# Optimization experiments

Hardware: AMD Instinct MI355X
Metric: run time of the kernel (lower is better)

## Reference

```python
import jax, jax.numpy as jnp
import numpy as np

# Channel layout assumed by the model's CH dict
CH_ELEV, CH_WS, CH_WD, CH_HUM, CH_NDVI, CH_FIRE = 0, 1, 2, 3, 4, 5
P_BURN, W_WIND, W_SLOPE = 0.58, 0.045, 0.078
OFFSETS = [(-1, 0), (-1, 1), (0, 1), (1, 1), (1, 0), (1, -1), (0, -1), (-1, -1)]
DIR_ANGLES = [90.0, 45.0, 0.0, 315.0, 270.0, 225.0, 180.0, 135.0]
SOBEL_X = np.array([[-1, 0, 1], [-2, 0, 2], [-1, 0, 1]], np.float32) / 8.0
SOBEL_Y = np.array([[-1, -2, -1], [0, 0, 0], [1, 2, 1]], np.float32) / 8.0


def setup_inputs() -> dict:
    key = jax.random.key(0)
    x = jax.random.uniform(key, (16, 6, 1024, 1024), dtype=jnp.float32)
    return {"x": x}


def _conv2d_same(img, k):
    # img: (B,1,H,W), k: (3,3)
    kern = jnp.asarray(k).reshape(1, 1, 3, 3)
    return jax.lax.conv_general_dilated(img, kern, (1, 1), ((1, 1), (1, 1)))


def _shift(mask, dr, dc):
    # mask: (B,H,W) float; zero-padded shift matching torch slicing
    B, H, W = mask.shape
    p = jnp.pad(mask, ((0, 0), (1, 1), (1, 1)))
    return p[:, 1 + dr:1 + dr + H, 1 + dc:1 + dc + W]


def reference(x):
    B, C, H, W = x.shape
    elev = x[:, CH_ELEV:CH_ELEV + 1]          # (B,1,H,W)
    ws = x[:, CH_WS]                           # (B,H,W)
    wd = x[:, CH_WD]
    hum = x[:, CH_HUM]
    ndvi = x[:, CH_NDVI]
    fs = x[:, CH_FIRE]

    dx = _conv2d_same(elev, SOBEL_X)
    dy = _conv2d_same(elev, SOBEL_Y)
    grad_mag = jnp.sqrt(dx * dx + dy * dy + 1e-8)
    slope = (jnp.arctan(grad_mag) * (180.0 / np.pi))[:, 0]  # (B,H,W) degrees

    burning = (fs > 0.5).astype(x.dtype)
    wind_math = jnp.mod(270.0 - wd, 360.0)
    slope_effect = 1.0 + W_SLOPE * jnp.tan(slope * (np.pi / 180.0))
    moisture_damp = jnp.clip(1.0 - 2.0 * hum * 200.0, 0.3, 1.0)
    veg_factor = 0.5 + 0.5 * jnp.clip(ndvi, 0.0, 1.0)
    base = P_BURN * slope_effect * moisture_damp * veg_factor  # wind-independent part

    prob = jnp.zeros((B, H, W), dtype=x.dtype)
    for (dr, dc), d_angle in zip(OFFSETS, DIR_ANGLES):
        shifted = _shift(burning, dr, dc)
        angle_diff = (d_angle - wind_math) * (np.pi / 180.0)
        wind_factor = 1.0 + W_WIND * jnp.cos(angle_diff) * ws
        p_spread = jnp.clip(base * wind_factor, 0.0, 1.0)
        prob = jnp.maximum(prob, shifted * p_spread)

    unburned = (fs < 0.5).astype(x.dtype)
    out = jnp.maximum(fs, prob * unburned)
    return out[:, None]  # (B,1,H,W)
```

## Files before the change

### kernel.cpp

```cpp
#include <hip/hip_runtime.h>

namespace {
constexpr int CH = 6;
constexpr int H  = 1024;
constexpr int W  = 1024;
constexpr float P_BURN  = 0.58f;
constexpr float W_WIND  = 0.045f;
constexpr float W_SLOPE = 0.078f;
constexpr float C45     = 0.70710678118654752f;
constexpr float DEG2RAD = 0.017453292519943295f;

__device__ __forceinline__ void load6(const float* __restrict__ plane, int row,
                                      int j0, float v[6]) {
    if ((unsigned)row >= (unsigned)H) {
        v[0] = v[1] = v[2] = v[3] = v[4] = v[5] = 0.f;
        return;
    }
    const float* r = plane + (size_t)row * W;
    const float4 m = *reinterpret_cast<const float4*>(r + j0);
    v[0] = (j0 > 0)     ? r[j0 - 1] : 0.f;
    v[1] = m.x; v[2] = m.y; v[3] = m.z; v[4] = m.w;
    v[5] = (j0 + 4 < W) ? r[j0 + 4] : 0.f;
}
}

__global__ __launch_bounds__(256)
void fire_step(const float* __restrict__ x, float* __restrict__ out, int B) {
    const int W4  = W / 4;
    const int gid = blockIdx.x * 256 + threadIdx.x;
    const int j0  = (gid % W4) * 4;
    const int rest = gid / W4;
    const int i = rest % H;
    const int b = rest / H;
    if (b >= B) return;

    const size_t plane = (size_t)H * W;
    const float* base_b = x + (size_t)b * CH * plane;
    const float* elev  = base_b + 0 * plane;
    const float* wsp   = base_b + 1 * plane;
    const float* wdp   = base_b + 2 * plane;
    const float* hump  = base_b + 3 * plane;
    const float* ndvip = base_b + 4 * plane;
    const float* fsp   = base_b + 5 * plane;

    float em[6], ec[6], ep[6];
    load6(elev, i - 1, j0, em);
    load6(elev, i,     j0, ec);
    load6(elev, i + 1, j0, ep);
    float fm[6], fc[6], fq[6];
    load6(fsp, i - 1, j0, fm);
    load6(fsp, i,     j0, fc);
    load6(fsp, i + 1, j0, fq);

    const size_t roff = (size_t)i * W + j0;
    const float4 ws4 = *reinterpret_cast<const float4*>(wsp   + roff);
    const float4 wd4 = *reinterpret_cast<const float4*>(wdp   + roff);
    const float4 hu4 = *reinterpret_cast<const float4*>(hump  + roff);
    const float4 nd4 = *reinterpret_cast<const float4*>(ndvip + roff);
    const float* wsa = reinterpret_cast<const float*>(&ws4);
    const float* wda = reinterpret_cast<const float*>(&wd4);
    const float* hua = reinterpret_cast<const float*>(&hu4);
    const float* nda = reinterpret_cast<const float*>(&nd4);

    float o[4];
#pragma unroll
    for (int k = 0; k < 4; ++k) {
        const float dx = ((em[k+2] - em[k]) + 2.f * (ec[k+2] - ec[k]) +
                          (ep[k+2] - ep[k])) * 0.125f;
        const float dy = ((ep[k]   - em[k]) + 2.f * (ep[k+1] - em[k+1]) +
                          (ep[k+2] - em[k+2])) * 0.125f;
        const float g = sqrtf(dx * dx + dy * dy + 1e-8f);
        const float slope_eff = 1.f + W_SLOPE * g;
        const float moist = fminf(fmaxf(1.f - 400.f * hua[k], 0.3f), 1.f);
        const float veg   = 0.5f + 0.5f * fminf(fmaxf(nda[k], 0.f), 1.f);
        const float basep = P_BURN * slope_eff * moist * veg;

        const float wrad = fmodf(270.f - wda[k], 360.f) * DEG2RAD;
        float sw, cw;
        __sincosf(wrad, &sw, &cw);

        float best = -2.f;
        if (fm[k+1] > 0.5f) best = fmaxf(best,  sw);
        if (fm[k+2] > 0.5f) best = fmaxf(best,  C45 * (cw + sw));
        if (fc[k+2] > 0.5f) best = fmaxf(best,  cw);
        if (fq[k+2] > 0.5f) best = fmaxf(best,  C45 * (cw - sw));
        if (fq[k+1] > 0.5f) best = fmaxf(best, -sw);
        if (fq[k]   > 0.5f) best = fmaxf(best, -C45 * (cw + sw));
        if (fc[k]   > 0.5f) best = fmaxf(best, -cw);
        if (fm[k]   > 0.5f) best = fmaxf(best,  C45 * (sw - cw));

        float prob = 0.f;
        if (best > -1.5f) {
            const float wf = 1.f + W_WIND * best * wsa[k];
            prob = fminf(fmaxf(basep * wf, 0.f), 1.f);
        }
        const float fsc = fc[k + 1];
        o[k] = fmaxf(fsc, (fsc < 0.5f) ? prob : 0.f);
    }

    float4 ov;
    ov.x = o[0]; ov.y = o[1]; ov.z = o[2]; ov.w = o[3];
    *reinterpret_cast<float4*>(out + (size_t)b * plane + roff) = ov;
}

extern "C" void kernel_launch(void* const* d_in, const int* in_sizes, int n_in,
                              void* d_out, int out_size, void* d_ws, size_t ws_size,
                              hipStream_t stream) {
    const float* x = (const float*)d_in[0];
    float* out = (float*)d_out;
    const int B = in_sizes[0] / (CH * H * W);
    const int total_threads = B * H * (W / 4);
    const int blocks = (total_threads + 255) / 256;
    fire_step<<<blocks, 256, 0, stream>>>(x, out, B);
}
```

Measured before the change: 526.2 us.

## Process four rows per thread with rolling stencil registers and XCD block swizzle

Each thread now computes four consecutive output rows and carries the elevation and fire-state rows forward in registers. This cuts the redundant global loads of the 3-row stencil from three rows per output row to about 1.5. Block indices are also remapped with an 8-way swizzle so that adjacent row groups land on the same XCD, which should improve L2 hit rates on halo rows. In exchange the grid has fewer blocks and each thread holds more registers.

```diff
diff --git a/kernel.cpp b/kernel.cpp
--- a/kernel.cpp
+++ b/kernel.cpp
@@ -4,6 +4,7 @@
 constexpr int CH = 6;
 constexpr int H  = 1024;
 constexpr int W  = 1024;
+constexpr int RPB = 4;
 constexpr float P_BURN  = 0.58f;
 constexpr float W_WIND  = 0.045f;
 constexpr float W_SLOPE = 0.078f;
@@ -26,13 +27,16 @@
 
 __global__ __launch_bounds__(256)
 void fire_step(const float* __restrict__ x, float* __restrict__ out, int B) {
-    const int W4  = W / 4;
-    const int gid = blockIdx.x * 256 + threadIdx.x;
-    const int j0  = (gid % W4) * 4;
-    const int rest = gid / W4;
-    const int i = rest % H;
-    const int b = rest / H;
+    const int nblk  = gridDim.x;
+    const int chunk = nblk >> 3;
+    const int bid   = blockIdx.x;
+    const int sbid  = (bid & 7) * chunk + (bid >> 3);
+
+    const int rgPerB = H / RPB;
+    const int b  = sbid / rgPerB;
+    const int r0 = (sbid % rgPerB) * RPB;
     if (b >= B) return;
+    const int j0 = (int)threadIdx.x * 4;
 
     const size_t plane = (size_t)H * W;
     const float* base_b = x + (size_t)b * CH * plane;
@@ -42,65 +46,77 @@
     const float* hump  = base_b + 3 * plane;
     const float* ndvip = base_b + 4 * plane;
     const float* fsp   = base_b + 5 * plane;
+    float* outp = out + (size_t)b * plane;
 
     float em[6], ec[6], ep[6];
-    load6(elev, i - 1, j0, em);
-    load6(elev, i,     j0, ec);
-    load6(elev, i + 1, j0, ep);
     float fm[6], fc[6], fq[6];
-    load6(fsp, i - 1, j0, fm);
-    load6(fsp, i,     j0, fc);
-    load6(fsp, i + 1, j0, fq);
+    load6(elev, r0 - 1, j0, em);
+    load6(elev, r0,     j0, ec);
+    load6(fsp,  r0 - 1, j0, fm);
+    load6(fsp,  r0,     j0, fc);
 
-    const size_t roff = (size_t)i * W + j0;
-    const float4 ws4 = *reinterpret_cast<const float4*>(wsp   + roff);
-    const float4 wd4 = *reinterpret_cast<const float4*>(wdp   + roff);
-    const float4 hu4 = *reinterpret_cast<const float4*>(hump  + roff);
-    const float4 nd4 = *reinterpret_cast<const float4*>(ndvip + roff);
-    const float* wsa = reinterpret_cast<const float*>(&ws4);
-    const float* wda = reinterpret_cast<const float*>(&wd4);
-    const float* hua = reinterpret_cast<const float*>(&hu4);
-    const float* nda = reinterpret_cast<const float*>(&nd4);
+#pragma unroll
+    for (int rr = 0; rr < RPB; ++rr) {
+        const int i = r0 + rr;
+        load6(elev, i + 1, j0, ep);
+        load6(fsp,  i + 1, j0, fq);
 
-    float o[4];
+        const size_t roff = (size_t)i * W + j0;
+        const float4 ws4 = *reinterpret_cast<const float4*>(wsp   + roff);
+        const float4 wd4 = *reinterpret_cast<const float4*>(wdp   + roff);
+        const float4 hu4 = *reinterpret_cast<const float4*>(hump  + roff);
+        const float4 nd4 = *reinterpret_cast<const float4*>(ndvip + roff);
+        const float* wsa = reinterpret_cast<const float*>(&ws4);
+        const float* wda = reinterpret_cast<const float*>(&wd4);
+        const float* hua = reinterpret_cast<const float*>(&hu4);
+        const float* nda = reinterpret_cast<const float*>(&nd4);
+
+        float o[4];
 #pragma unroll
-    for (int k = 0; k < 4; ++k) {
-        const float dx = ((em[k+2] - em[k]) + 2.f * (ec[k+2] - ec[k]) +
-                          (ep[k+2] - ep[k])) * 0.125f;
-        const float dy = ((ep[k]   - em[k]) + 2.f * (ep[k+1] - em[k+1]) +
-                          (ep[k+2] - em[k+2])) * 0.125f;
-        const float g = sqrtf(dx * dx + dy * dy + 1e-8f);
-        const float slope_eff = 1.f + W_SLOPE * g;
-        const float moist = fminf(fmaxf(1.f - 400.f * hua[k], 0.3f), 1.f);
-        const float veg   = 0.5f + 0.5f * fminf(fmaxf(nda[k], 0.f), 1.f);
-        const float basep = P_BURN * slope_eff * moist * veg;
+        for (int k = 0; k < 4; ++k) {
+            const float dx = ((em[k+2] - em[k]) + 2.f * (ec[k+2] - ec[k]) +
+                              (ep[k+2] - ep[k])) * 0.125f;
+            const float dy = ((ep[k]   - em[k]) + 2.f * (ep[k+1] - em[k+1]) +
+                              (ep[k+2] - em[k+2])) * 0.125f;
+            const float g = sqrtf(dx * dx + dy * dy + 1e-8f);
+            const float slope_eff = 1.f + W_SLOPE * g;
+            const float moist = fminf(fmaxf(1.f - 400.f * hua[k], 0.3f), 1.f);
+            const float veg   = 0.5f + 0.5f * fminf(fmaxf(nda[k], 0.f), 1.f);
+            const float basep = P_BURN * slope_eff * moist * veg;
 
-        const float wrad = fmodf(270.f - wda[k], 360.f) * DEG2RAD;
-        float sw, cw;
-        __sincosf(wrad, &sw, &cw);
+            const float wrad = fmodf(270.f - wda[k], 360.f) * DEG2RAD;
+            float sw, cw;
+            __sincosf(wrad, &sw, &cw);
 
-        float best = -2.f;
-        if (fm[k+1] > 0.5f) best = fmaxf(best,  sw);
-        if (fm[k+2] > 0.5f) best = fmaxf(best,  C45 * (cw + sw));
-        if (fc[k+2] > 0.5f) best = fmaxf(best,  cw);
-        if (fq[k+2] > 0.5f) best = fmaxf(best,  C45 * (cw - sw));
-        if (fq[k+1] > 0.5f) best = fmaxf(best, -sw);
-        if (fq[k]   > 0.5f) best = fmaxf(best, -C45 * (cw + sw));
-        if (fc[k]   > 0.5f) best = fmaxf(best, -cw);
-        if (fm[k]   > 0.5f) best = fmaxf(best,  C45 * (sw - cw));
+            float best = -2.f;
+            if (fm[k+1] > 0.5f) best = fmaxf(best,  sw);
+            if (fm[k+2] > 0.5f) best = fmaxf(best,  C45 * (cw + sw));
+            if (fc[k+2] > 0.5f) best = fmaxf(best,  cw);
+            if (fq[k+2] > 0.5f) best = fmaxf(best,  C45 * (cw - sw));
+            if (fq[k+1] > 0.5f) best = fmaxf(best, -sw);
+            if (fq[k]   > 0.5f) best = fmaxf(best, -C45 * (cw + sw));
+            if (fc[k]   > 0.5f) best = fmaxf(best, -cw);
+            if (fm[k]   > 0.5f) best = fmaxf(best,  C45 * (sw - cw));
 
-        float prob = 0.f;
-        if (best > -1.5f) {
-            const float wf = 1.f + W_WIND * best * wsa[k];
-            prob = fminf(fmaxf(basep * wf, 0.f), 1.f);
+            float prob = 0.f;
+            if (best > -1.5f) {
+                const float wf = 1.f + W_WIND * best * wsa[k];
+                prob = fminf(fmaxf(basep * wf, 0.f), 1.f);
+            }
+            const float fsc = fc[k + 1];
+            o[k] = fmaxf(fsc, (fsc < 0.5f) ? prob : 0.f);
         }
-        const float fsc = fc[k + 1];
-        o[k] = fmaxf(fsc, (fsc < 0.5f) ? prob : 0.f);
+
+        float4 ov;
+        ov.x = o[0]; ov.y = o[1]; ov.z = o[2]; ov.w = o[3];
+        *reinterpret_cast<float4*>(outp + roff) = ov;
+
+#pragma unroll
+        for (int t = 0; t < 6; ++t) {
+            em[t] = ec[t]; ec[t] = ep[t];
+            fm[t] = fc[t]; fc[t] = fq[t];
+        }
     }
-
-    float4 ov;
-    ov.x = o[0]; ov.y = o[1]; ov.z = o[2]; ov.w = o[3];
-    *reinterpret_cast<float4*>(out + (size_t)b * plane + roff) = ov;
 }
 
 extern "C" void kernel_launch(void* const* d_in, const int* in_sizes, int n_in,
@@ -109,7 +125,6 @@
     const float* x = (const float*)d_in[0];
     float* out = (float*)d_out;
     const int B = in_sizes[0] / (CH * H * W);
-    const int total_threads = B * H * (W / 4);
-    const int blocks = (total_threads + 255) / 256;
+    const int blocks = B * (H / RPB);
     fire_step<<<blocks, 256, 0, stream>>>(x, out, B);
 }
```

Result: slower. 554.5 us (+5.4%).
